# Optimization experiments

Hardware: AMD Instinct MI355X
Metric: run time of the kernel (lower is better)

## Reference

```python
import jax, jax.numpy as jnp
import numpy as np

B, N, K = 128, 1000, 10  # queries, docs per query, NDCG cutoff (hard-coded k=10 in module)


def setup_inputs() -> dict:
    key = jax.random.key(0)
    k1, k2 = jax.random.split(key)
    predictions = jax.random.normal(k1, (B, N), dtype=jnp.float32)
    labels = jax.random.randint(k2, (B, N), 0, 5).astype(jnp.float32)  # graded relevance 0..4
    return {"predictions": predictions, "labels": labels}


def _ndcg_loss(predictions, rel, k=K):
    # relevance gathered in descending-score order, top-k only
    order = jnp.argsort(-predictions, axis=-1)[:, :k]            # [B, k]
    rel_by_score = jnp.take_along_axis(rel, order, axis=-1)      # [B, k]
    ideal_rel, _ = jax.lax.top_k(rel, k)                          # [B, k] sorted desc
    denoms = jnp.log2(jnp.arange(k, dtype=jnp.float32) + 2.0)    # [k]
    dcg = jnp.sum(rel_by_score / denoms, axis=-1)                # [B]
    idcg = jnp.sum(ideal_rel / denoms, axis=-1)                  # [B]
    return jnp.sum(1.0 - dcg / idcg)


def reference(predictions, labels):
    rel = jnp.power(2.0, labels) - 1.0
    return _ndcg_loss(predictions, rel)
```

## Files before the change

### kernel.cpp

```cpp
#include <hip/hip_runtime.h>
#include <stdint.h>

#define B_QUERIES 128
#define N_DOCS    1000
#define NVEC      250
#define K_TOP     10
#define ROWS_PER_BLOCK 4

__device__ __forceinline__ uint32_t f32_sortable(float f) {
    uint32_t u = __float_as_uint(f);
    return (u & 0x80000000u) ? ~u : (u | 0x80000000u);
}

__device__ __forceinline__ double pack_key(float p, int idx, int li) {
    uint64_t kb = 0x4000000000000000ull
                | ((uint64_t)f32_sortable(p) << 13)
                | ((uint64_t)(uint32_t)(1023 - idx) << 3)
                | (uint64_t)(uint32_t)li;
    return __longlong_as_double((long long)kb);
}

template<int CTRL, int RMASK>
__device__ __forceinline__ double dpp_mov_f64(double x) {
    uint64_t u = (uint64_t)__double_as_longlong(x);
    uint32_t lo = (uint32_t)__builtin_amdgcn_update_dpp(0, (int)(uint32_t)u,         CTRL, RMASK, 0xf, false);
    uint32_t hi = (uint32_t)__builtin_amdgcn_update_dpp(0, (int)(uint32_t)(u >> 32), CTRL, RMASK, 0xf, false);
    return __longlong_as_double((long long)(((uint64_t)hi << 32) | lo));
}

__device__ __forceinline__ double wave_max_f64_bcast(double x) {
    x = fmax(x, dpp_mov_f64<0x111, 0xf>(x));
    x = fmax(x, dpp_mov_f64<0x112, 0xf>(x));
    x = fmax(x, dpp_mov_f64<0x114, 0xf>(x));
    x = fmax(x, dpp_mov_f64<0x118, 0xf>(x));
    x = fmax(x, dpp_mov_f64<0x142, 0xa>(x));
    x = fmax(x, dpp_mov_f64<0x143, 0xc>(x));
    uint64_t u = (uint64_t)__double_as_longlong(x);
    uint32_t lo = (uint32_t)__builtin_amdgcn_readlane((int)(uint32_t)u,         63);
    uint32_t hi = (uint32_t)__builtin_amdgcn_readlane((int)(uint32_t)(u >> 32), 63);
    return __longlong_as_double((long long)(((uint64_t)hi << 32) | lo));
}

template<int CTRL, int RMASK>
__device__ __forceinline__ uint64_t dpp_mov_u64(uint64_t x) {
    uint32_t lo = (uint32_t)__builtin_amdgcn_update_dpp(0, (int)(uint32_t)x,         CTRL, RMASK, 0xf, false);
    uint32_t hi = (uint32_t)__builtin_amdgcn_update_dpp(0, (int)(uint32_t)(x >> 32), CTRL, RMASK, 0xf, false);
    return ((uint64_t)hi << 32) | lo;
}

__device__ __forceinline__ uint64_t wave_sum_u64_bcast(uint64_t x) {
    x += dpp_mov_u64<0x111, 0xf>(x);
    x += dpp_mov_u64<0x112, 0xf>(x);
    x += dpp_mov_u64<0x114, 0xf>(x);
    x += dpp_mov_u64<0x118, 0xf>(x);
    x += dpp_mov_u64<0x142, 0xa>(x);
    x += dpp_mov_u64<0x143, 0xc>(x);
    uint32_t lo = (uint32_t)__builtin_amdgcn_readlane((int)(uint32_t)x,         63);
    uint32_t hi = (uint32_t)__builtin_amdgcn_readlane((int)(uint32_t)(x >> 32), 63);
    return ((uint64_t)hi << 32) | lo;
}

template<int CTRL, int RMASK>
__device__ __forceinline__ float dpp_mov_f32(float x) {
    return __int_as_float(__builtin_amdgcn_update_dpp(0, __float_as_int(x), CTRL, RMASK, 0xf, false));
}

__device__ __forceinline__ float wave_sum_f32_bcast(float x) {
    x += dpp_mov_f32<0x111, 0xf>(x);
    x += dpp_mov_f32<0x112, 0xf>(x);
    x += dpp_mov_f32<0x114, 0xf>(x);
    x += dpp_mov_f32<0x118, 0xf>(x);
    x += dpp_mov_f32<0x142, 0xa>(x);
    x += dpp_mov_f32<0x143, 0xc>(x);
    return __int_as_float(__builtin_amdgcn_readlane(__float_as_int(x), 63));
}

__global__ __launch_bounds__(ROWS_PER_BLOCK * 64) void ndcg_fused_kernel(
        const float* __restrict__ pred,
        const float* __restrict__ lab,
        float* __restrict__ out) {
    const int wave = threadIdx.x >> 6;
    const int lane = threadIdx.x & 63;
    const int row  = blockIdx.x * ROWS_PER_BLOCK + wave;
    const float4* p4 = (const float4*)(pred + row * N_DOCS);
    const float4* l4 = (const float4*)(lab  + row * N_DOCS);

    const float inv_denom[K_TOP] = {
        1.0f, 0.63092977f, 0.5f, 0.43067656f, 0.38685282f,
        0.35620719f, 0.33333334f, 0.31546488f, 0.30102998f, 0.28906483f
    };

    double key[16];
    uint64_t h = 0;

    #pragma unroll
    for (int j = 0; j < 4; ++j) {
        int v = lane + j * 64;
        bool act = (v < NVEC);
        float4 pv = act ? p4[v] : make_float4(0.f, 0.f, 0.f, 0.f);
        float4 lv = act ? l4[v] : make_float4(0.f, 0.f, 0.f, 0.f);
        float pp[4] = {pv.x, pv.y, pv.z, pv.w};
        float ll[4] = {lv.x, lv.y, lv.z, lv.w};
        #pragma unroll
        for (int c = 0; c < 4; ++c) {
            int idx = v * 4 + c;
            int li  = (int)(ll[c] + 0.5f);
            key[j * 4 + c] = act ? pack_key(pp[c], idx, li) : 0.0;
            if (act && li > 0) h += 1ull << ((li - 1) * 16);
        }
    }

    h = wave_sum_u64_bcast(h);

    int c4 = (int)((h >> 48) & 0xFFFFull);
    int c3 = (int)((h >> 32) & 0xFFFFull);
    int c2 = (int)((h >> 16) & 0xFFFFull);
    int c1 = (int)( h        & 0xFFFFull);
    int cum4 = c4, cum3 = cum4 + c3, cum2 = cum3 + c2, cum1 = cum2 + c1;
    float contrib = 0.0f;
    if (lane < K_TOP) {
        float rel = lane < cum4 ? 15.0f
                  : lane < cum3 ?  7.0f
                  : lane < cum2 ?  3.0f
                  : lane < cum1 ?  1.0f : 0.0f;
        contrib = rel * __builtin_amdgcn_rcpf(__log2f((float)(lane + 2)));
    }
    float idcg = wave_sum_f32_bcast(contrib);

    float dcg = 0.0f;
    double lastKey;
    {
        double m[16];
        #pragma unroll
        for (int jj = 0; jj < 16; ++jj) m[jj] = key[jj];
        #pragma unroll
        for (int s = 8; s > 0; s >>= 1)
            #pragma unroll
            for (int jj = 0; jj < s; ++jj) m[jj] = fmax(m[jj], m[jj + s]);
        double best = wave_max_f64_bcast(m[0]);
        lastKey = best;
        int lv = (int)((uint64_t)__double_as_longlong(best) & 0x7ull);
        dcg += (float)((1 << lv) - 1) * inv_denom[0];
    }
    #pragma unroll
    for (int r = 1; r < K_TOP; ++r) {
        double m[16];
        #pragma unroll
        for (int jj = 0; jj < 16; ++jj)
            m[jj] = (key[jj] < lastKey) ? key[jj] : 0.0;
        #pragma unroll
        for (int s = 8; s > 0; s >>= 1)
            #pragma unroll
            for (int jj = 0; jj < s; ++jj) m[jj] = fmax(m[jj], m[jj + s]);
        double best = wave_max_f64_bcast(m[0]);
        lastKey = best;
        int lv = (int)((uint64_t)__double_as_longlong(best) & 0x7ull);
        dcg += (float)((1 << lv) - 1) * inv_denom[r];
    }

    __shared__ float part[ROWS_PER_BLOCK];
    if (lane == 0) part[wave] = 1.0f - dcg / idcg;
    __syncthreads();
    if (threadIdx.x == 0) {
        float s = part[0] + part[1] + part[2] + part[3];
        atomicAdd(out, s);
    }
}

extern "C" void kernel_launch(void* const* d_in, const int* in_sizes, int n_in,
                              void* d_out, int out_size, void* d_ws, size_t ws_size,
                              hipStream_t stream) {
    (void)in_sizes; (void)n_in; (void)out_size; (void)d_ws; (void)ws_size;
    const float* pred = (const float*)d_in[0];
    const float* lab  = (const float*)d_in[1];
    float* out = (float*)d_out;

    ndcg_fused_kernel<<<B_QUERIES / ROWS_PER_BLOCK, ROWS_PER_BLOCK * 64, 0, stream>>>(pred, lab, out);
}
```

Baseline: 57.75 us.

## Sort per-lane keys once and pop lane heads for top-k selection

Each lane's 16 packed keys are sorted once with a Batcher odd-even merge network, and only the top 10 are kept. Each of the 10 selection rounds then takes a wave-wide max of every lane's head element, and the winning lane shifts its list. Before, every round filtered and max-reduced all 16 keys against the previous winner. The selection rounds get much cheaper in exchange for a one-time sorting network of about 60 compare-exchanges on doubles, plus a shift step in each round.

```diff
diff --git a/kernel.cpp b/kernel.cpp
--- a/kernel.cpp
+++ b/kernel.cpp
@@ -127,35 +127,44 @@
     }
     float idcg = wave_sum_f32_bcast(contrib);
 
+    #pragma unroll
+    for (int p = 1; p < 16; p <<= 1) {
+        #pragma unroll
+        for (int k = p; k >= 1; k >>= 1) {
+            #pragma unroll
+            for (int j = k & (p - 1); j + k < 16; j += 2 * k) {
+                #pragma unroll
+                for (int i = 0; i < k; ++i) {
+                    if (i + j + k < 16 &&
+                        (i + j) / (2 * p) == (i + j + k) / (2 * p)) {
+                        int a = i + j, b = i + j + k;
+                        double hi = fmax(key[a], key[b]);
+                        double lo = fmin(key[a], key[b]);
+                        key[a] = hi;
+                        key[b] = lo;
+                    }
+                }
+            }
+        }
+    }
+
+    double sk[K_TOP];
+    #pragma unroll
+    for (int i = 0; i < K_TOP; ++i) sk[i] = key[i];
+
     float dcg = 0.0f;
-    double lastKey;
-    {
-        double m[16];
-        #pragma unroll
-        for (int jj = 0; jj < 16; ++jj) m[jj] = key[jj];
-        #pragma unroll
-        for (int s = 8; s > 0; s >>= 1)
-            #pragma unroll
-            for (int jj = 0; jj < s; ++jj) m[jj] = fmax(m[jj], m[jj + s]);
-        double best = wave_max_f64_bcast(m[0]);
-        lastKey = best;
-        int lv = (int)((uint64_t)__double_as_longlong(best) & 0x7ull);
-        dcg += (float)((1 << lv) - 1) * inv_denom[0];
-    }
     #pragma unroll
-    for (int r = 1; r < K_TOP; ++r) {
-        double m[16];
-        #pragma unroll
-        for (int jj = 0; jj < 16; ++jj)
-            m[jj] = (key[jj] < lastKey) ? key[jj] : 0.0;
-        #pragma unroll
-        for (int s = 8; s > 0; s >>= 1)
-            #pragma unroll
-            for (int jj = 0; jj < s; ++jj) m[jj] = fmax(m[jj], m[jj + s]);
-        double best = wave_max_f64_bcast(m[0]);
-        lastKey = best;
+    for (int r = 0; r < K_TOP; ++r) {
+        double best = wave_max_f64_bcast(sk[0]);
         int lv = (int)((uint64_t)__double_as_longlong(best) & 0x7ull);
         dcg += (float)((1 << lv) - 1) * inv_denom[r];
+        if (r < K_TOP - 1) {
+            bool win = (sk[0] == best);
+            #pragma unroll
+            for (int i = 0; i < K_TOP - 1; ++i)
+                sk[i] = win ? sk[i + 1] : sk[i];
+            sk[K_TOP - 1] = win ? 0.0 : sk[K_TOP - 1];
+        }
     }
 
     __shared__ float part[ROWS_PER_BLOCK];
```

Result: no change. 57.56 us (-0.3%).
